# Kernel optimization log

Measured on AMD Instinct MI355X. Metric: run time of the kernel, lower is better.

## Reference

```python
import jax, jax.numpy as jnp
import numpy as np

TOP_K = 48
NUM_RBF = 16
MAX_REL = 32  # max_relative_feature
B, L = 2, 3072

# atom order in stacked tensor: N=0, Ca=1, C=2, O=3, Cb=4
_PAIRS = np.array([
    (0, 0), (2, 2), (3, 3), (4, 4), (1, 0), (1, 2), (1, 3), (1, 4),
    (0, 2), (0, 3), (0, 4), (4, 2), (4, 3), (3, 2), (0, 1), (2, 1),
    (3, 1), (4, 1), (2, 0), (3, 0), (4, 0), (2, 4), (3, 4), (2, 3)], dtype=np.int32)


def _rbf(D):
    # D [..., ] -> [..., NUM_RBF]
    mu = jnp.linspace(2.0, 22.0, NUM_RBF)
    sigma = (22.0 - 2.0) / NUM_RBF
    return jnp.exp(-(((D[..., None] - mu) / sigma) ** 2))


def setup_inputs() -> dict:
    key = jax.random.key(0)
    ks = jax.random.split(key, 8)
    X = jax.random.normal(ks[0], (B, L, 4, 3), dtype=jnp.float32) * 3.0
    mask = jnp.ones((B, L), dtype=jnp.float32)
    R_idx = jnp.sort(jax.random.randint(ks[1], (B, L), 0, 6144), axis=-1)
    chain_labels = jax.random.randint(ks[2], (B, L), 0, 4)
    pos_W = jax.random.normal(ks[3], (2 * MAX_REL + 2, 16), dtype=jnp.float32) * 0.1
    pos_b = jax.random.normal(ks[4], (16,), dtype=jnp.float32) * 0.02
    edge_W = jax.random.normal(ks[5], (16 + 25 * NUM_RBF, 128), dtype=jnp.float32) * 0.05
    ln_gamma = jnp.ones((128,), dtype=jnp.float32)
    ln_beta = jnp.zeros((128,), dtype=jnp.float32)
    return {"X": X, "mask": mask, "R_idx": R_idx, "chain_labels": chain_labels,
            "pos_W": pos_W, "pos_b": pos_b, "edge_W": edge_W,
            "ln_gamma": ln_gamma, "ln_beta": ln_beta}


def reference(X, mask, R_idx, chain_labels, pos_W, pos_b, edge_W, ln_gamma, ln_beta):
    # virtual Cb construction
    bvec = X[:, :, 1, :] - X[:, :, 0, :]
    cvec = X[:, :, 2, :] - X[:, :, 1, :]
    avec = jnp.cross(bvec, cvec)
    Ca = X[:, :, 1, :]
    Cb = -0.58273431 * avec + 0.56802827 * bvec - 0.54067466 * cvec + Ca
    atoms = jnp.stack([X[:, :, 0, :], Ca, X[:, :, 2, :], X[:, :, 3, :], Cb], axis=2)  # [B,L,5,3]

    # masked pairwise Ca distances + k smallest neighbors
    mask2d = mask[:, :, None] * mask[:, None, :]                        # [B,L,L]
    dX = Ca[:, :, None, :] - Ca[:, None, :, :]
    D = mask2d * jnp.sqrt(jnp.sum(dX ** 2, axis=-1) + 1e-6)
    D_max = jnp.max(D, axis=-1, keepdims=True)
    D_adjust = D + (1.0 - mask2d) * D_max
    k = min(TOP_K, X.shape[1])
    neg_vals, E_idx = jax.lax.top_k(-D_adjust, k)                       # [B,L,K]
    D_neighbors = -neg_vals

    # gather neighbor atom coords once: [B,L,K,5,3]
    atoms_nb = jax.vmap(lambda a, i: a[i])(atoms, E_idx)

    # 24 remaining atom-pair distances, restricted to neighbors (same math as
    # full cdist + gather since dist is computed per (i, E_idx[i,j]) pair)
    ai, bi = _PAIRS[:, 0], _PAIRS[:, 1]
    diff = atoms[:, :, None, ai, :] - atoms_nb[:, :, :, bi, :]          # [B,L,K,24,3]
    D24 = jnp.sqrt(jnp.sum(diff ** 2, axis=-1) + 1e-6)                  # [B,L,K,24]

    D_all = jnp.concatenate([D_neighbors[..., None], D24], axis=-1)    # [B,L,K,25]
    RBF_all = _rbf(D_all).reshape(D_all.shape[:3] + (25 * NUM_RBF,))   # [B,L,K,400]

    # positional encodings on neighbor offsets
    offset = R_idx[:, :, None] - R_idx[:, None, :]
    offset = jnp.take_along_axis(offset, E_idx, axis=2)                 # [B,L,K]
    same_chain = (chain_labels[:, :, None] - chain_labels[:, None, :] == 0).astype(jnp.int32)
    E_chains = jnp.take_along_axis(same_chain, E_idx, axis=2)           # [B,L,K]
    d = jnp.clip(offset + MAX_REL, 0, 2 * MAX_REL) * E_chains + (1 - E_chains) * (2 * MAX_REL + 1)
    E_positional = pos_W[d] + pos_b                                     # one-hot @ W == row gather

    E = jnp.concatenate([E_positional, RBF_all], axis=-1)              # [B,L,K,416]
    E = E @ edge_W                                                      # [B,L,K,128]
    mu = jnp.mean(E, axis=-1, keepdims=True)
    var = jnp.mean((E - mu) ** 2, axis=-1, keepdims=True)
    E = (E - mu) / jnp.sqrt(var + 1e-5) * ln_gamma + ln_beta
    return E, E_idx
```

## Files before the change

### kernel.cpp

```cpp
#include <hip/hip_runtime.h>
#include <hip/hip_bf16.h>
#include <stdint.h>
#include <math.h>

#define B_   2
#define L_   3072
#define K_   48
#define FDIM 416
#define NOUT 128
#define FRS8 424
#define NLUT 1920

__device__ const unsigned char PAIRC[24] = {
    0, 18, 27, 36, 8, 10, 11, 12, 2, 3, 4, 34, 35, 26,
    1, 17, 25, 33, 16, 24, 32, 20, 28, 19
};

typedef __attribute__((ext_vector_type(4))) float f32x4;

__global__ __launch_bounds__(256) void k_prep(const float* __restrict__ X,
                                              const float* __restrict__ mask,
                                              const float* __restrict__ edgeW,
                                              float* __restrict__ atoms,
                                              float* __restrict__ CaA4,
                                              unsigned char* __restrict__ Wt8,
                                              uint4* __restrict__ LUT)
{
    const int bid = blockIdx.x;
    if (bid < 52) {
        int idx4 = bid * 256 + threadIdx.x;
        int b = idx4 * 4;
        int lhi = (b >> 3) & 3;
        int l15 = (b >> 5) & 15;
        int nt  = (b >> 9) & 7;
        int kt  = b >> 12;
        int n = (nt >> 1) * 32 + 2 * l15 + (nt & 1);
        int kbase = kt * 32 + lhi * 8 + (b & 7);
        float v0 = edgeW[(kbase + 0) * NOUT + n];
        float v1 = edgeW[(kbase + 1) * NOUT + n];
        float v2 = edgeW[(kbase + 2) * NOUT + n];
        float v3 = edgeW[(kbase + 3) * NOUT + n];
        int w = __builtin_amdgcn_cvt_pk_fp8_f32(v0, v1, 0, false);
        w = __builtin_amdgcn_cvt_pk_fp8_f32(v2, v3, w, true);
        ((unsigned int*)Wt8)[idx4] = (unsigned int)w;
    } else if (bid < 60) {
        int e = (bid - 52) * 256 + threadIdx.x;
        if (e >= NLUT) return;
        float D = (float)e * 0.015625f;
        float z = (D - 2.0f) * 0.8f;
        unsigned int u[4];
        #pragma unroll
        for (int p = 0; p < 4; ++p) {
            float e0 = __expf(-(z * z)); z -= 1.0666667f;
            float e1 = __expf(-(z * z)); z -= 1.0666667f;
            float e2 = __expf(-(z * z)); z -= 1.0666667f;
            float e3 = __expf(-(z * z)); z -= 1.0666667f;
            int w = __builtin_amdgcn_cvt_pk_fp8_f32(e0, e1, 0, false);
            w = __builtin_amdgcn_cvt_pk_fp8_f32(e2, e3, w, true);
            u[p] = (unsigned int)w;
        }
        LUT[e] = make_uint4(u[0], u[1], u[2], u[3]);
    } else {
        int row = (bid - 60) * 256 + threadIdx.x;
        if (row >= B_ * L_) return;
        const float* x = X + row * 12;
        float nx = x[0], ny = x[1], nz = x[2];
        float cax = x[3], cay = x[4], caz = x[5];
        float cx = x[6], cy = x[7], cz = x[8];
        float ox = x[9], oy = x[10], oz = x[11];
        float bx = cax - nx, by = cay - ny, bz = caz - nz;
        float vx = cx - cax, vy = cy - cay, vz = cz - caz;
        float axv = by * vz - bz * vy;
        float ayv = bz * vx - bx * vz;
        float azv = bx * vy - by * vx;
        float cbx = -0.58273431f * axv + 0.56802827f * bx - 0.54067466f * vx + cax;
        float cby = -0.58273431f * ayv + 0.56802827f * by - 0.54067466f * vy + cay;
        float cbz = -0.58273431f * azv + 0.56802827f * bz - 0.54067466f * vz + caz;
        float* A = atoms + row * 16;
        A[0] = nx;  A[1] = ny;  A[2] = nz;
        A[3] = cax; A[4] = cay; A[5] = caz;
        A[6] = cx;  A[7] = cy;  A[8] = cz;
        A[9] = ox;  A[10] = oy; A[11] = oz;
        A[12] = cbx; A[13] = cby; A[14] = cbz;
        A[15] = 0.f;
        float4 c4 = make_float4(cax, cay, caz, mask[row]);
        *(float4*)(CaA4 + row * 4) = c4;
    }
}

__global__ __launch_bounds__(256) void k_topk(const float* __restrict__ CaA4,
                                              int* __restrict__ eidx,
                                              float* __restrict__ dnb,
                                              float* __restrict__ out_eidx_f)
{
    __shared__ __align__(16) unsigned int SH[3072];
    unsigned int* hist  = SH;
    unsigned int* candJ = SH + 2048;
    unsigned long long* candK = (unsigned long long*)SH;
    __shared__ unsigned int swave[4];
    __shared__ int sP;
    __shared__ unsigned int sCnt;

    const int row = blockIdx.x;
    const int b = row / L_;
    const int tid = threadIdx.x;
    const int lane = tid & 63;
    const int wv = tid >> 6;

    #pragma unroll
    for (int i = 0; i < 8; ++i) hist[tid + 256 * i] = 0;
    if (tid == 0) sCnt = 0;

    const float4 me = *(const float4*)(CaA4 + row * 4);
    const float4* Cb = (const float4*)(CaA4 + (size_t)b * L_ * 4);
    __syncthreads();

    unsigned int bits[12];
    #pragma unroll
    for (int m = 0; m < 12; ++m) {
        int j = tid + 256 * m;
        float4 nb = Cb[j];
        float dx = me.x - nb.x;
        float dy = me.y - nb.y;
        float dz = me.z - nb.z;
        float s = fmaf(dz, dz, fmaf(dy, dy, dx * dx)) + 1e-6f;
        bool live = (me.w * nb.w) != 0.0f;
        bits[m] = live ? __float_as_uint(s) : 0x7F800000u;
        atomicAdd(&hist[bits[m] >> 20], 1u);
    }
    __syncthreads();

    unsigned int loc[8];
    unsigned int s = 0;
    #pragma unroll
    for (int i = 0; i < 8; ++i) { loc[i] = hist[tid * 8 + i]; s += loc[i]; }
    unsigned int sc = s;
    #pragma unroll
    for (int off = 1; off < 64; off <<= 1) {
        unsigned int o = __shfl_up(sc, off);
        if (lane >= off) sc += o;
    }
    if (lane == 63) swave[wv] = sc;
    __syncthreads();
    unsigned int base = 0;
    #pragma unroll
    for (int w = 0; w < 4; ++w) if (w < wv) base += swave[w];
    unsigned int cum = base + sc - s;
    #pragma unroll
    for (int i = 0; i < 8; ++i) {
        unsigned int c = loc[i];
        if (cum < K_ && cum + c >= K_) sP = tid * 8 + i;
        cum += c;
    }
    __syncthreads();
    const unsigned int Pth = (unsigned int)sP + 2;

    #pragma unroll
    for (int m = 0; m < 12; ++m) {
        if ((bits[m] >> 20) <= Pth) {
            unsigned int pos = atomicAdd(&sCnt, 1u);
            if (pos < 1024) candJ[pos] = (unsigned)(tid + 256 * m);
        }
    }
    __syncthreads();
    int cnt = (int)sCnt;
    if (cnt > 1024) cnt = 1024;

    const double cax = (double)me.x, cay = (double)me.y, caz = (double)me.z;
    for (int i = tid; i < cnt; i += 256) {
        int j = (int)candJ[i];
        float4 nb = Cb[j];
        double dx = cax - (double)nb.x;
        double dy = cay - (double)nb.y;
        double dz = caz - (double)nb.z;
        double ss = dx * dx;
        ss = ss + dy * dy;
        ss = ss + dz * dz;
        ss = ss + 1e-6;
        float v = (float)sqrt(ss);
        candK[i] = ((unsigned long long)__float_as_uint(v) << 32) | (unsigned)j;
    }
    __syncthreads();

    if (cnt <= 64) {
        if (wv == 0) {
            unsigned long long k = (lane < cnt) ? candK[lane] : ~0ull;
            #pragma unroll
            for (int size = 2; size <= 64; size <<= 1) {
                #pragma unroll
                for (int stride = size >> 1; stride >= 1; stride >>= 1) {
                    unsigned long long o = __shfl_xor(k, stride);
                    bool low = (lane & stride) == 0;
                    bool up = (lane & size) == 0 || size == 64;
                    unsigned long long mn = k < o ? k : o;
                    unsigned long long mx = k < o ? o : k;
                    k = (low == up) ? mn : mx;
                }
            }
            if (lane < K_) {
                int gj = (int)(unsigned)(k & 0xffffffffu);
                eidx[row * K_ + lane] = gj;
                dnb[row * K_ + lane] = __uint_as_float((unsigned)(k >> 32));
                out_eidx_f[row * K_ + lane] = (float)gj;
            }
        }
    } else {
        int M2 = 128;
        while (M2 < cnt) M2 <<= 1;
        for (int i = cnt + tid; i < M2; i += 256) candK[i] = ~0ull;
        for (int size = 2; size <= M2; size <<= 1) {
            for (int stride = size >> 1; stride > 0; stride >>= 1) {
                __syncthreads();
                for (int i = tid; i < M2; i += 256) {
                    int p = i ^ stride;
                    if (p > i) {
                        unsigned long long a = candK[i];
                        unsigned long long c2 = candK[p];
                        bool up = ((i & size) == 0);
                        if ((a > c2) == up) { candK[i] = c2; candK[p] = a; }
                    }
                }
            }
        }
        __syncthreads();
        if (tid < K_) {
            unsigned long long g = candK[tid];
            int gj = (int)(unsigned)(g & 0xffffffffu);
            eidx[row * K_ + tid] = gj;
            dnb[row * K_ + tid] = __uint_as_float((unsigned)(g >> 32));
            out_eidx_f[row * K_ + tid] = (float)gj;
        }
    }
}

__global__ __launch_bounds__(256) void k_edge(const float* __restrict__ atoms,
                                              const int* __restrict__ eidx,
                                              const float* __restrict__ dnb,
                                              const int* __restrict__ Ridx,
                                              const int* __restrict__ chain,
                                              const float* __restrict__ posW,
                                              const float* __restrict__ posb,
                                              const unsigned char* __restrict__ Wt8,
                                              const uint4* __restrict__ LUT,
                                              const float* __restrict__ gamma,
                                              const float* __restrict__ beta,
                                              float* __restrict__ Eout)
{
    __shared__ __align__(16) unsigned char F8[K_ * FRS8];
    __shared__ __align__(16) float sOwn[16];
    __shared__ int   sE[K_];
    __shared__ float sDnb[K_];
    __shared__ int   sDpos[K_];
    __shared__ float Psum[K_][4];
    __shared__ float Psq[K_][4];

    const int row = blockIdx.x;
    const int b = row / L_;
    const int tid = threadIdx.x;

    if (tid < K_) {
        int j = eidx[row * K_ + tid];
        sE[tid] = j;
        sDnb[tid] = dnb[row * K_ + tid];
        int off = Ridx[row] - Ridx[b * L_ + j];
        int ch = (chain[row] == chain[b * L_ + j]) ? 1 : 0;
        sDpos[tid] = ch ? min(max(off + 32, 0), 64) : 65;
    } else if (tid < K_ + 4) {
        int part = tid - K_;
        *(float4*)(&sOwn[part * 4]) = *(const float4*)(atoms + (size_t)row * 16 + part * 4);
    }
    __syncthreads();

    if (tid < 240) {
        const int k = tid / 5;
        const int dd0 = tid - k * 5;
        const float* pj = atoms + ((size_t)b * L_ + sE[k]) * 16;
        unsigned char* Fk = F8 + k * FRS8;
        #pragma unroll
        for (int s5 = 0; s5 < 5; ++s5) {
            const int dd = dd0 + 5 * s5;
            float D;
            if (dd == 0) {
                D = sDnb[k];
            } else {
                int pr = PAIRC[dd - 1];
                int ai = pr >> 3, bi = pr & 7;
                float dx = sOwn[ai * 3 + 0] - pj[bi * 3 + 0];
                float dy = sOwn[ai * 3 + 1] - pj[bi * 3 + 1];
                float dz = sOwn[ai * 3 + 2] - pj[bi * 3 + 2];
                D = sqrtf(fmaf(dz, dz, fmaf(dy, dy, dx * dx)) + 1e-6f);
            }
            float Dc = fminf(D, 29.984375f);
            int idx = (int)fmaf(Dc, 64.0f, 0.5f);
            uint4 v = LUT[idx];
            *(uint4*)(Fk + 16 + dd * 16) = v;
        }
    }
    for (int s2 = tid; s2 < K_ * 16; s2 += 256) {
        int k = s2 >> 4, r = s2 & 15;
        float v = posW[sDpos[k] * 16 + r] + posb[r];
        int w = __builtin_amdgcn_cvt_pk_fp8_f32(v, v, 0, false);
        F8[k * FRS8 + r] = (unsigned char)(w & 0xff);
    }
    __syncthreads();

    const int lane = tid & 63;
    const int wv = tid >> 6;
    const int l15 = lane & 15;
    const int lhi = lane >> 4;

    f32x4 acc[3][2];
    #pragma unroll
    for (int mt = 0; mt < 3; ++mt)
        #pragma unroll
        for (int nn = 0; nn < 2; ++nn)
            acc[mt][nn] = (f32x4){0.f, 0.f, 0.f, 0.f};

    const unsigned char* wp = Wt8 + wv * 1024 + l15 * 32 + lhi * 8;
    long bc0 = *(const long*)(wp);
    long bc1 = *(const long*)(wp + 512);

    #pragma unroll 1
    for (int kt = 0; kt < 13; ++kt) {
        long bn0 = 0, bn1 = 0;
        if (kt < 12) {
            bn0 = *(const long*)(wp + (kt + 1) * 4096);
            bn1 = *(const long*)(wp + (kt + 1) * 4096 + 512);
        }
        const int k0 = kt * 32 + lhi * 8;
        long a0 = *(const long*)(F8 + (l15) * FRS8 + k0);
        long a1 = *(const long*)(F8 + (16 + l15) * FRS8 + k0);
        long a2 = *(const long*)(F8 + (32 + l15) * FRS8 + k0);
        acc[0][0] = __builtin_amdgcn_mfma_f32_16x16x32_fp8_fp8(a0, bc0, acc[0][0], 0, 0, 0);
        acc[0][1] = __builtin_amdgcn_mfma_f32_16x16x32_fp8_fp8(a0, bc1, acc[0][1], 0, 0, 0);
        acc[1][0] = __builtin_amdgcn_mfma_f32_16x16x32_fp8_fp8(a1, bc0, acc[1][0], 0, 0, 0);
        acc[1][1] = __builtin_amdgcn_mfma_f32_16x16x32_fp8_fp8(a1, bc1, acc[1][1], 0, 0, 0);
        acc[2][0] = __builtin_amdgcn_mfma_f32_16x16x32_fp8_fp8(a2, bc0, acc[2][0], 0, 0, 0);
        acc[2][1] = __builtin_amdgcn_mfma_f32_16x16x32_fp8_fp8(a2, bc1, acc[2][1], 0, 0, 0);
        bc0 = bn0;
        bc1 = bn1;
    }

    #pragma unroll
    for (int mt = 0; mt < 3; ++mt) {
        #pragma unroll
        for (int r = 0; r < 4; ++r) {
            float v0 = acc[mt][0][r], v1 = acc[mt][1][r];
            float sv = v0 + v1;
            float q = v0 * v0 + v1 * v1;
            #pragma unroll
            for (int off = 1; off < 16; off <<= 1) {
                sv += __shfl_xor(sv, off);
                q += __shfl_xor(q, off);
            }
            if (l15 == 0) {
                int er = mt * 16 + lhi * 4 + r;
                Psum[er][wv] = sv;
                Psq[er][wv] = q;
            }
        }
    }
    __syncthreads();

    const int c0p = wv * 32 + 2 * l15;
    float2 g2 = *(const float2*)(gamma + c0p);
    float2 b2 = *(const float2*)(beta + c0p);

    #pragma unroll
    for (int mt = 0; mt < 3; ++mt) {
        #pragma unroll
        for (int r = 0; r < 4; ++r) {
            int er = mt * 16 + lhi * 4 + r;
            float sv = Psum[er][0] + Psum[er][1] + Psum[er][2] + Psum[er][3];
            float q = Psq[er][0] + Psq[er][1] + Psq[er][2] + Psq[er][3];
            float mu = sv * (1.0f / 128.0f);
            float var = q * (1.0f / 128.0f) - mu * mu;
            float inv = 1.0f / sqrtf(var + 1e-5f);
            float2 o;
            o.x = (acc[mt][0][r] - mu) * inv * g2.x + b2.x;
            o.y = (acc[mt][1][r] - mu) * inv * g2.y + b2.y;
            *(float2*)(Eout + ((size_t)row * K_ + er) * 128 + c0p) = o;
        }
    }
}

extern "C" void kernel_launch(void* const* d_in, const int* in_sizes, int n_in,
                              void* d_out, int out_size, void* d_ws, size_t ws_size,
                              hipStream_t stream) {
    const float* X     = (const float*)d_in[0];
    const float* mask  = (const float*)d_in[1];
    const int*   Ridx  = (const int*)d_in[2];
    const int*   chain = (const int*)d_in[3];
    const float* posW  = (const float*)d_in[4];
    const float* posb  = (const float*)d_in[5];
    const float* edgeW = (const float*)d_in[6];
    const float* gamma = (const float*)d_in[7];
    const float* beta  = (const float*)d_in[8];

    float* out   = (float*)d_out;
    float* Eout  = out;
    float* EidxF = out + (size_t)B_ * L_ * K_ * NOUT;

    float* atoms = (float*)d_ws;
    float* CaA4  = atoms + (size_t)B_ * L_ * 16;
    int*   eidx  = (int*)(CaA4 + (size_t)B_ * L_ * 4);
    float* dnb   = (float*)(eidx + (size_t)B_ * L_ * K_);
    unsigned char* Wt8 = (unsigned char*)(dnb + (size_t)B_ * L_ * K_);
    uint4* LUT   = (uint4*)(Wt8 + 53248);

    hipLaunchKernelGGL(k_prep, dim3(60 + (B_ * L_ + 255) / 256), dim3(256), 0, stream,
                       X, mask, edgeW, atoms, CaA4, Wt8, LUT);
    hipLaunchKernelGGL(k_topk, dim3(B_ * L_), dim3(256), 0, stream,
                       CaA4, eidx, dnb, EidxF);
    hipLaunchKernelGGL(k_edge, dim3(B_ * L_), dim3(256), 0, stream,
                       atoms, eidx, dnb, Ridx, chain, posW, posb, Wt8, LUT, gamma, beta, Eout);
}
```

Baseline: 121.0 us.

## Process two rows per block in top-k and edge kernels

Both the top-k and edge kernels now handle two query rows per 256-thread block, halving the grid. In top-k, each loaded neighbour coordinate is reused for two distance computations and two histograms. In the edge kernel, each fp8 weight fragment loaded from global memory feeds six MFMA row tiles instead of three, halving weight traffic per row. The cost is more registers and shared memory per block, which may lower occupancy, and the candidate buffer per row shrinks from 1024 to 768 entries.

```diff
diff --git a/kernel.cpp b/kernel.cpp
--- a/kernel.cpp
+++ b/kernel.cpp
@@ -93,142 +93,197 @@
                                               float* __restrict__ dnb,
                                               float* __restrict__ out_eidx_f)
 {
-    __shared__ __align__(16) unsigned int SH[3072];
-    unsigned int* hist  = SH;
-    unsigned int* candJ = SH + 2048;
-    unsigned long long* candK = (unsigned long long*)SH;
+    __shared__ __align__(16) unsigned int SH[5632];
     __shared__ unsigned int swave[4];
-    __shared__ int sP;
-    __shared__ unsigned int sCnt;
-
-    const int row = blockIdx.x;
-    const int b = row / L_;
+    __shared__ int sP[2];
+    __shared__ unsigned int sCnt[2];
+
+    const int row0 = blockIdx.x * 2;
+    const int row1 = row0 + 1;
+    const int b = row0 / L_;
     const int tid = threadIdx.x;
     const int lane = tid & 63;
     const int wv = tid >> 6;
 
     #pragma unroll
-    for (int i = 0; i < 8; ++i) hist[tid + 256 * i] = 0;
-    if (tid == 0) sCnt = 0;
-
-    const float4 me = *(const float4*)(CaA4 + row * 4);
+    for (int i = 0; i < 16; ++i) SH[tid + 256 * i] = 0;
+    if (tid < 2) sCnt[tid] = 0;
+
+    const float4 me0 = *(const float4*)(CaA4 + row0 * 4);
+    const float4 me1 = *(const float4*)(CaA4 + row1 * 4);
     const float4* Cb = (const float4*)(CaA4 + (size_t)b * L_ * 4);
     __syncthreads();
 
-    unsigned int bits[12];
+    unsigned int bits0[12], bits1[12];
     #pragma unroll
     for (int m = 0; m < 12; ++m) {
         int j = tid + 256 * m;
         float4 nb = Cb[j];
-        float dx = me.x - nb.x;
-        float dy = me.y - nb.y;
-        float dz = me.z - nb.z;
-        float s = fmaf(dz, dz, fmaf(dy, dy, dx * dx)) + 1e-6f;
-        bool live = (me.w * nb.w) != 0.0f;
-        bits[m] = live ? __float_as_uint(s) : 0x7F800000u;
-        atomicAdd(&hist[bits[m] >> 20], 1u);
-    }
-    __syncthreads();
-
-    unsigned int loc[8];
-    unsigned int s = 0;
-    #pragma unroll
-    for (int i = 0; i < 8; ++i) { loc[i] = hist[tid * 8 + i]; s += loc[i]; }
-    unsigned int sc = s;
-    #pragma unroll
-    for (int off = 1; off < 64; off <<= 1) {
-        unsigned int o = __shfl_up(sc, off);
-        if (lane >= off) sc += o;
-    }
-    if (lane == 63) swave[wv] = sc;
-    __syncthreads();
-    unsigned int base = 0;
-    #pragma unroll
-    for (int w = 0; w < 4; ++w) if (w < wv) base += swave[w];
-    unsigned int cum = base + sc - s;
-    #pragma unroll
-    for (int i = 0; i < 8; ++i) {
-        unsigned int c = loc[i];
-        if (cum < K_ && cum + c >= K_) sP = tid * 8 + i;
-        cum += c;
-    }
-    __syncthreads();
-    const unsigned int Pth = (unsigned int)sP + 2;
-
+        float dx0 = me0.x - nb.x, dy0 = me0.y - nb.y, dz0 = me0.z - nb.z;
+        float s0 = fmaf(dz0, dz0, fmaf(dy0, dy0, dx0 * dx0)) + 1e-6f;
+        bits0[m] = ((me0.w * nb.w) != 0.0f) ? __float_as_uint(s0) : 0x7F800000u;
+        float dx1 = me1.x - nb.x, dy1 = me1.y - nb.y, dz1 = me1.z - nb.z;
+        float s1 = fmaf(dz1, dz1, fmaf(dy1, dy1, dx1 * dx1)) + 1e-6f;
+        bits1[m] = ((me1.w * nb.w) != 0.0f) ? __float_as_uint(s1) : 0x7F800000u;
+        atomicAdd(&SH[bits0[m] >> 20], 1u);
+        atomicAdd(&SH[2048 + (bits1[m] >> 20)], 1u);
+    }
+    __syncthreads();
+
+    #pragma unroll
+    for (int r2 = 0; r2 < 2; ++r2) {
+        unsigned int loc[8];
+        unsigned int s = 0;
+        #pragma unroll
+        for (int i = 0; i < 8; ++i) { loc[i] = SH[r2 * 2048 + tid * 8 + i]; s += loc[i]; }
+        unsigned int sc = s;
+        #pragma unroll
+        for (int off = 1; off < 64; off <<= 1) {
+            unsigned int o = __shfl_up(sc, off);
+            if (lane >= off) sc += o;
+        }
+        if (lane == 63) swave[wv] = sc;
+        __syncthreads();
+        unsigned int base = 0;
+        #pragma unroll
+        for (int w = 0; w < 4; ++w) if (w < wv) base += swave[w];
+        unsigned int cum = base + sc - s;
+        #pragma unroll
+        for (int i = 0; i < 8; ++i) {
+            unsigned int c = loc[i];
+            if (cum < K_ && cum + c >= K_) sP[r2] = tid * 8 + i;
+            cum += c;
+        }
+        __syncthreads();
+    }
+    const unsigned int Pth0 = (unsigned int)sP[0] + 2;
+    const unsigned int Pth1 = (unsigned int)sP[1] + 2;
+
+    unsigned int* candJ = SH + 4096;
     #pragma unroll
     for (int m = 0; m < 12; ++m) {
-        if ((bits[m] >> 20) <= Pth) {
-            unsigned int pos = atomicAdd(&sCnt, 1u);
-            if (pos < 1024) candJ[pos] = (unsigned)(tid + 256 * m);
-        }
-    }
-    __syncthreads();
-    int cnt = (int)sCnt;
-    if (cnt > 1024) cnt = 1024;
-
-    const double cax = (double)me.x, cay = (double)me.y, caz = (double)me.z;
-    for (int i = tid; i < cnt; i += 256) {
-        int j = (int)candJ[i];
-        float4 nb = Cb[j];
-        double dx = cax - (double)nb.x;
-        double dy = cay - (double)nb.y;
-        double dz = caz - (double)nb.z;
-        double ss = dx * dx;
-        ss = ss + dy * dy;
-        ss = ss + dz * dz;
-        ss = ss + 1e-6;
-        float v = (float)sqrt(ss);
-        candK[i] = ((unsigned long long)__float_as_uint(v) << 32) | (unsigned)j;
-    }
-    __syncthreads();
-
-    if (cnt <= 64) {
-        if (wv == 0) {
-            unsigned long long k = (lane < cnt) ? candK[lane] : ~0ull;
+        if ((bits0[m] >> 20) <= Pth0) {
+            unsigned int pos = atomicAdd(&sCnt[0], 1u);
+            if (pos < 768) candJ[pos] = (unsigned)(tid + 256 * m);
+        }
+        if ((bits1[m] >> 20) <= Pth1) {
+            unsigned int pos = atomicAdd(&sCnt[1], 1u);
+            if (pos < 768) candJ[768 + pos] = (unsigned)(tid + 256 * m);
+        }
+    }
+    __syncthreads();
+    int cnt0 = (int)sCnt[0]; if (cnt0 > 768) cnt0 = 768;
+    int cnt1 = (int)sCnt[1]; if (cnt1 > 768) cnt1 = 768;
+
+    unsigned long long* candK = (unsigned long long*)SH;
+    {
+        const double cax = (double)me0.x, cay = (double)me0.y, caz = (double)me0.z;
+        for (int i = tid; i < cnt0; i += 256) {
+            int j = (int)candJ[i];
+            float4 nb = Cb[j];
+            double dx = cax - (double)nb.x;
+            double dy = cay - (double)nb.y;
+            double dz = caz - (double)nb.z;
+            double ss = dx * dx;
+            ss = ss + dy * dy;
+            ss = ss + dz * dz;
+            ss = ss + 1e-6;
+            float v = (float)sqrt(ss);
+            candK[i] = ((unsigned long long)__float_as_uint(v) << 32) | (unsigned)j;
+        }
+    }
+    {
+        const double cax = (double)me1.x, cay = (double)me1.y, caz = (double)me1.z;
+        for (int i = tid; i < cnt1; i += 256) {
+            int j = (int)candJ[768 + i];
+            float4 nb = Cb[j];
+            double dx = cax - (double)nb.x;
+            double dy = cay - (double)nb.y;
+            double dz = caz - (double)nb.z;
+            double ss = dx * dx;
+            ss = ss + dy * dy;
+            ss = ss + dz * dz;
+            ss = ss + 1e-6;
+            float v = (float)sqrt(ss);
+            candK[1024 + i] = ((unsigned long long)__float_as_uint(v) << 32) | (unsigned)j;
+        }
+    }
+    __syncthreads();
+
+    const bool small0 = (cnt0 <= 64), small1 = (cnt1 <= 64);
+    if (small0 && wv == 0) {
+        unsigned long long k = (lane < cnt0) ? candK[lane] : ~0ull;
+        #pragma unroll
+        for (int size = 2; size <= 64; size <<= 1) {
             #pragma unroll
-            for (int size = 2; size <= 64; size <<= 1) {
-                #pragma unroll
-                for (int stride = size >> 1; stride >= 1; stride >>= 1) {
-                    unsigned long long o = __shfl_xor(k, stride);
-                    bool low = (lane & stride) == 0;
-                    bool up = (lane & size) == 0 || size == 64;
-                    unsigned long long mn = k < o ? k : o;
-                    unsigned long long mx = k < o ? o : k;
-                    k = (low == up) ? mn : mx;
-                }
-            }
-            if (lane < K_) {
-                int gj = (int)(unsigned)(k & 0xffffffffu);
-                eidx[row * K_ + lane] = gj;
-                dnb[row * K_ + lane] = __uint_as_float((unsigned)(k >> 32));
-                out_eidx_f[row * K_ + lane] = (float)gj;
-            }
-        }
-    } else {
+            for (int stride = size >> 1; stride >= 1; stride >>= 1) {
+                unsigned long long o = __shfl_xor(k, stride);
+                bool low = (lane & stride) == 0;
+                bool up = (lane & size) == 0 || size == 64;
+                unsigned long long mn = k < o ? k : o;
+                unsigned long long mx = k < o ? o : k;
+                k = (low == up) ? mn : mx;
+            }
+        }
+        if (lane < K_) {
+            int gj = (int)(unsigned)(k & 0xffffffffu);
+            eidx[row0 * K_ + lane] = gj;
+            dnb[row0 * K_ + lane] = __uint_as_float((unsigned)(k >> 32));
+            out_eidx_f[row0 * K_ + lane] = (float)gj;
+        }
+    }
+    if (small1 && wv == 1) {
+        unsigned long long k = (lane < cnt1) ? candK[1024 + lane] : ~0ull;
+        #pragma unroll
+        for (int size = 2; size <= 64; size <<= 1) {
+            #pragma unroll
+            for (int stride = size >> 1; stride >= 1; stride >>= 1) {
+                unsigned long long o = __shfl_xor(k, stride);
+                bool low = (lane & stride) == 0;
+                bool up = (lane & size) == 0 || size == 64;
+                unsigned long long mn = k < o ? k : o;
+                unsigned long long mx = k < o ? o : k;
+                k = (low == up) ? mn : mx;
+            }
+        }
+        if (lane < K_) {
+            int gj = (int)(unsigned)(k & 0xffffffffu);
+            eidx[row1 * K_ + lane] = gj;
+            dnb[row1 * K_ + lane] = __uint_as_float((unsigned)(k >> 32));
+            out_eidx_f[row1 * K_ + lane] = (float)gj;
+        }
+    }
+    #pragma unroll
+    for (int r2 = 0; r2 < 2; ++r2) {
+        int cnt = r2 ? cnt1 : cnt0;
+        bool small = r2 ? small1 : small0;
+        if (small) continue;
+        unsigned long long* ck = candK + r2 * 1024;
+        int rowg = r2 ? row1 : row0;
         int M2 = 128;
         while (M2 < cnt) M2 <<= 1;
-        for (int i = cnt + tid; i < M2; i += 256) candK[i] = ~0ull;
+        for (int i = cnt + tid; i < M2; i += 256) ck[i] = ~0ull;
         for (int size = 2; size <= M2; size <<= 1) {
             for (int stride = size >> 1; stride > 0; stride >>= 1) {
                 __syncthreads();
                 for (int i = tid; i < M2; i += 256) {
                     int p = i ^ stride;
                     if (p > i) {
-                        unsigned long long a = candK[i];
-                        unsigned long long c2 = candK[p];
+                        unsigned long long a = ck[i];
+                        unsigned long long c2 = ck[p];
                         bool up = ((i & size) == 0);
-                        if ((a > c2) == up) { candK[i] = c2; candK[p] = a; }
+                        if ((a > c2) == up) { ck[i] = c2; ck[p] = a; }
                     }
                 }
             }
         }
         __syncthreads();
         if (tid < K_) {
-            unsigned long long g = candK[tid];
+            unsigned long long g = ck[tid];
             int gj = (int)(unsigned)(g & 0xffffffffu);
-            eidx[row * K_ + tid] = gj;
-            dnb[row * K_ + tid] = __uint_as_float((unsigned)(g >> 32));
-            out_eidx_f[row * K_ + tid] = (float)gj;
+            eidx[rowg * K_ + tid] = gj;
+            dnb[rowg * K_ + tid] = __uint_as_float((unsigned)(g >> 32));
+            out_eidx_f[rowg * K_ + tid] = (float)gj;
         }
     }
 }
@@ -246,61 +301,70 @@
                                               const float* __restrict__ beta,
                                               float* __restrict__ Eout)
 {
-    __shared__ __align__(16) unsigned char F8[K_ * FRS8];
-    __shared__ __align__(16) float sOwn[16];
-    __shared__ int   sE[K_];
-    __shared__ float sDnb[K_];
-    __shared__ int   sDpos[K_];
-    __shared__ float Psum[K_][4];
-    __shared__ float Psq[K_][4];
-
-    const int row = blockIdx.x;
-    const int b = row / L_;
+    __shared__ __align__(16) unsigned char F8[96 * FRS8];
+    __shared__ __align__(16) float sOwn[2][16];
+    __shared__ int   sE[96];
+    __shared__ float sDnb[96];
+    __shared__ int   sDpos[96];
+    __shared__ float Psum[96][4];
+    __shared__ float Psq[96][4];
+
+    const int row0 = blockIdx.x * 2;
+    const int b = row0 / L_;
     const int tid = threadIdx.x;
 
-    if (tid < K_) {
-        int j = eidx[row * K_ + tid];
+    if (tid < 96) {
+        int r2 = (tid >= 48) ? 1 : 0;
+        int row = row0 + r2;
+        int kl = tid - r2 * 48;
+        int j = eidx[row * K_ + kl];
         sE[tid] = j;
-        sDnb[tid] = dnb[row * K_ + tid];
+        sDnb[tid] = dnb[row * K_ + kl];
         int off = Ridx[row] - Ridx[b * L_ + j];
         int ch = (chain[row] == chain[b * L_ + j]) ? 1 : 0;
         sDpos[tid] = ch ? min(max(off + 32, 0), 64) : 65;
-    } else if (tid < K_ + 4) {
-        int part = tid - K_;
-        *(float4*)(&sOwn[part * 4]) = *(const float4*)(atoms + (size_t)row * 16 + part * 4);
+    } else if (tid < 104) {
+        int part = tid - 96;
+        int r2 = part >> 2;
+        *(float4*)(&sOwn[r2][(part & 3) * 4]) =
+            *(const float4*)(atoms + (size_t)(row0 + r2) * 16 + (part & 3) * 4);
     }
     __syncthreads();
 
     if (tid < 240) {
         const int k = tid / 5;
         const int dd0 = tid - k * 5;
-        const float* pj = atoms + ((size_t)b * L_ + sE[k]) * 16;
-        unsigned char* Fk = F8 + k * FRS8;
-        #pragma unroll
-        for (int s5 = 0; s5 < 5; ++s5) {
-            const int dd = dd0 + 5 * s5;
-            float D;
-            if (dd == 0) {
-                D = sDnb[k];
-            } else {
-                int pr = PAIRC[dd - 1];
-                int ai = pr >> 3, bi = pr & 7;
-                float dx = sOwn[ai * 3 + 0] - pj[bi * 3 + 0];
-                float dy = sOwn[ai * 3 + 1] - pj[bi * 3 + 1];
-                float dz = sOwn[ai * 3 + 2] - pj[bi * 3 + 2];
-                D = sqrtf(fmaf(dz, dz, fmaf(dy, dy, dx * dx)) + 1e-6f);
-            }
-            float Dc = fminf(D, 29.984375f);
-            int idx = (int)fmaf(Dc, 64.0f, 0.5f);
-            uint4 v = LUT[idx];
-            *(uint4*)(Fk + 16 + dd * 16) = v;
-        }
-    }
-    for (int s2 = tid; s2 < K_ * 16; s2 += 256) {
-        int k = s2 >> 4, r = s2 & 15;
-        float v = posW[sDpos[k] * 16 + r] + posb[r];
+        #pragma unroll
+        for (int r2 = 0; r2 < 2; ++r2) {
+            const int e = r2 * 48 + k;
+            const float* pj = atoms + ((size_t)b * L_ + sE[e]) * 16;
+            unsigned char* Fk = F8 + e * FRS8;
+            #pragma unroll
+            for (int s5 = 0; s5 < 5; ++s5) {
+                const int dd = dd0 + 5 * s5;
+                float D;
+                if (dd == 0) {
+                    D = sDnb[e];
+                } else {
+                    int pr = PAIRC[dd - 1];
+                    int ai = pr >> 3, bi = pr & 7;
+                    float dx = sOwn[r2][ai * 3 + 0] - pj[bi * 3 + 0];
+                    float dy = sOwn[r2][ai * 3 + 1] - pj[bi * 3 + 1];
+                    float dz = sOwn[r2][ai * 3 + 2] - pj[bi * 3 + 2];
+                    D = sqrtf(fmaf(dz, dz, fmaf(dy, dy, dx * dx)) + 1e-6f);
+                }
+                float Dc = fminf(D, 29.984375f);
+                int idx = (int)fmaf(Dc, 64.0f, 0.5f);
+                uint4 v = LUT[idx];
+                *(uint4*)(Fk + 16 + dd * 16) = v;
+            }
+        }
+    }
+    for (int s2 = tid; s2 < 96 * 16; s2 += 256) {
+        int e = s2 >> 4, r = s2 & 15;
+        float v = posW[sDpos[e] * 16 + r] + posb[r];
         int w = __builtin_amdgcn_cvt_pk_fp8_f32(v, v, 0, false);
-        F8[k * FRS8 + r] = (unsigned char)(w & 0xff);
+        F8[e * FRS8 + r] = (unsigned char)(w & 0xff);
     }
     __syncthreads();
 
@@ -309,9 +373,9 @@
     const int l15 = lane & 15;
     const int lhi = lane >> 4;
 
-    f32x4 acc[3][2];
-    #pragma unroll
-    for (int mt = 0; mt < 3; ++mt)
+    f32x4 acc[6][2];
+    #pragma unroll
+    for (int mt = 0; mt < 6; ++mt)
         #pragma unroll
         for (int nn = 0; nn < 2; ++nn)
             acc[mt][nn] = (f32x4){0.f, 0.f, 0.f, 0.f};
@@ -328,21 +392,18 @@
             bn1 = *(const long*)(wp + (kt + 1) * 4096 + 512);
         }
         const int k0 = kt * 32 + lhi * 8;
-        long a0 = *(const long*)(F8 + (l15) * FRS8 + k0);
-        long a1 = *(const long*)(F8 + (16 + l15) * FRS8 + k0);
-        long a2 = *(const long*)(F8 + (32 + l15) * FRS8 + k0);
-        acc[0][0] = __builtin_amdgcn_mfma_f32_16x16x32_fp8_fp8(a0, bc0, acc[0][0], 0, 0, 0);
-        acc[0][1] = __builtin_amdgcn_mfma_f32_16x16x32_fp8_fp8(a0, bc1, acc[0][1], 0, 0, 0);
-        acc[1][0] = __builtin_amdgcn_mfma_f32_16x16x32_fp8_fp8(a1, bc0, acc[1][0], 0, 0, 0);
-        acc[1][1] = __builtin_amdgcn_mfma_f32_16x16x32_fp8_fp8(a1, bc1, acc[1][1], 0, 0, 0);
-        acc[2][0] = __builtin_amdgcn_mfma_f32_16x16x32_fp8_fp8(a2, bc0, acc[2][0], 0, 0, 0);
-        acc[2][1] = __builtin_amdgcn_mfma_f32_16x16x32_fp8_fp8(a2, bc1, acc[2][1], 0, 0, 0);
+        #pragma unroll
+        for (int mt = 0; mt < 6; ++mt) {
+            long a = *(const long*)(F8 + (mt * 16 + l15) * FRS8 + k0);
+            acc[mt][0] = __builtin_amdgcn_mfma_f32_16x16x32_fp8_fp8(a, bc0, acc[mt][0], 0, 0, 0);
+            acc[mt][1] = __builtin_amdgcn_mfma_f32_16x16x32_fp8_fp8(a, bc1, acc[mt][1], 0, 0, 0);
+        }
         bc0 = bn0;
         bc1 = bn1;
     }
 
     #pragma unroll
-    for (int mt = 0; mt < 3; ++mt) {
+    for (int mt = 0; mt < 6; ++mt) {
         #pragma unroll
         for (int r = 0; r < 4; ++r) {
             float v0 = acc[mt][0][r], v1 = acc[mt][1][r];
@@ -367,7 +428,7 @@
     float2 b2 = *(const float2*)(beta + c0p);
 
     #pragma unroll
-    for (int mt = 0; mt < 3; ++mt) {
+    for (int mt = 0; mt < 6; ++mt) {
         #pragma unroll
         for (int r = 0; r < 4; ++r) {
             int er = mt * 16 + lhi * 4 + r;
@@ -376,10 +437,12 @@
             float mu = sv * (1.0f / 128.0f);
             float var = q * (1.0f / 128.0f) - mu * mu;
             float inv = 1.0f / sqrtf(var + 1e-5f);
+            int row = row0 + (er >= 48 ? 1 : 0);
+            int kl = er & 47;
             float2 o;
             o.x = (acc[mt][0][r] - mu) * inv * g2.x + b2.x;
             o.y = (acc[mt][1][r] - mu) * inv * g2.y + b2.y;
-            *(float2*)(Eout + ((size_t)row * K_ + er) * 128 + c0p) = o;
+            *(float2*)(Eout + ((size_t)row * K_ + kl) * 128 + c0p) = o;
         }
     }
 }
@@ -410,8 +473,8 @@
 
     hipLaunchKernelGGL(k_prep, dim3(60 + (B_ * L_ + 255) / 256), dim3(256), 0, stream,
                        X, mask, edgeW, atoms, CaA4, Wt8, LUT);
-    hipLaunchKernelGGL(k_topk, dim3(B_ * L_), dim3(256), 0, stream,
+    hipLaunchKernelGGL(k_topk, dim3(B_ * L_ / 2), dim3(256), 0, stream,
                        CaA4, eidx, dnb, EidxF);
-    hipLaunchKernelGGL(k_edge, dim3(B_ * L_), dim3(256), 0, stream,
+    hipLaunchKernelGGL(k_edge, dim3(B_ * L_ / 2), dim3(256), 0, stream,
                        atoms, eidx, dnb, Ridx, chain, posW, posb, Wt8, LUT, gamma, beta, Eout);
 }
```

New measurement: 160.6 us. 1.33x slower.

## Split edge GEMM over eight waves with one N-tile per wave

Applied to the files above, without the earlier changes.

Doubles the k_edge block to 512 threads so each of eight waves computes a single 16-column output tile instead of two, halving per-wave accumulators and weight loads. Feature construction is respread over 480 threads, and the LayerNorm partial sums now reduce across eight waves. Output stores shrink from float2 to scalar with interleaved columns, which may hurt store coalescing. The intent is more latency hiding per row, at the cost of more synchronisation and shared-memory reduction work.

```diff
diff --git a/kernel.cpp b/kernel.cpp
--- a/kernel.cpp
+++ b/kernel.cpp
@@ -233,7 +233,7 @@
     }
 }
 
-__global__ __launch_bounds__(256) void k_edge(const float* __restrict__ atoms,
+__global__ __launch_bounds__(512) void k_edge(const float* __restrict__ atoms,
                                               const int* __restrict__ eidx,
                                               const float* __restrict__ dnb,
                                               const int* __restrict__ Ridx,
@@ -251,8 +251,8 @@
     __shared__ int   sE[K_];
     __shared__ float sDnb[K_];
     __shared__ int   sDpos[K_];
-    __shared__ float Psum[K_][4];
-    __shared__ float Psq[K_][4];
+    __shared__ float Psum[K_][8];
+    __shared__ float Psq[K_][8];
 
     const int row = blockIdx.x;
     const int b = row / L_;
@@ -271,14 +271,15 @@
     }
     __syncthreads();
 
-    if (tid < 240) {
-        const int k = tid / 5;
-        const int dd0 = tid - k * 5;
+    if (tid < 480) {
+        const int k = tid / 10;
+        const int dd0 = tid - k * 10;
         const float* pj = atoms + ((size_t)b * L_ + sE[k]) * 16;
         unsigned char* Fk = F8 + k * FRS8;
         #pragma unroll
-        for (int s5 = 0; s5 < 5; ++s5) {
-            const int dd = dd0 + 5 * s5;
+        for (int s3 = 0; s3 < 3; ++s3) {
+            const int dd = dd0 + 10 * s3;
+            if (dd >= 25) break;
             float D;
             if (dd == 0) {
                 D = sDnb[k];
@@ -296,7 +297,7 @@
             *(uint4*)(Fk + 16 + dd * 16) = v;
         }
     }
-    for (int s2 = tid; s2 < K_ * 16; s2 += 256) {
+    for (int s2 = tid; s2 < K_ * 16; s2 += 512) {
         int k = s2 >> 4, r = s2 & 15;
         float v = posW[sDpos[k] * 16 + r] + posb[r];
         int w = __builtin_amdgcn_cvt_pk_fp8_f32(v, v, 0, false);
@@ -309,45 +310,35 @@
     const int l15 = lane & 15;
     const int lhi = lane >> 4;
 
-    f32x4 acc[3][2];
+    f32x4 acc[3];
     #pragma unroll
     for (int mt = 0; mt < 3; ++mt)
-        #pragma unroll
-        for (int nn = 0; nn < 2; ++nn)
-            acc[mt][nn] = (f32x4){0.f, 0.f, 0.f, 0.f};
-
-    const unsigned char* wp = Wt8 + wv * 1024 + l15 * 32 + lhi * 8;
-    long bc0 = *(const long*)(wp);
-    long bc1 = *(const long*)(wp + 512);
+        acc[mt] = (f32x4){0.f, 0.f, 0.f, 0.f};
+
+    const unsigned char* wp = Wt8 + wv * 512 + l15 * 32 + lhi * 8;
+    long bc = *(const long*)(wp);
 
     #pragma unroll 1
     for (int kt = 0; kt < 13; ++kt) {
-        long bn0 = 0, bn1 = 0;
-        if (kt < 12) {
-            bn0 = *(const long*)(wp + (kt + 1) * 4096);
-            bn1 = *(const long*)(wp + (kt + 1) * 4096 + 512);
-        }
+        long bn = 0;
+        if (kt < 12) bn = *(const long*)(wp + (kt + 1) * 4096);
         const int k0 = kt * 32 + lhi * 8;
         long a0 = *(const long*)(F8 + (l15) * FRS8 + k0);
         long a1 = *(const long*)(F8 + (16 + l15) * FRS8 + k0);
         long a2 = *(const long*)(F8 + (32 + l15) * FRS8 + k0);
-        acc[0][0] = __builtin_amdgcn_mfma_f32_16x16x32_fp8_fp8(a0, bc0, acc[0][0], 0, 0, 0);
-        acc[0][1] = __builtin_amdgcn_mfma_f32_16x16x32_fp8_fp8(a0, bc1, acc[0][1], 0, 0, 0);
-        acc[1][0] = __builtin_amdgcn_mfma_f32_16x16x32_fp8_fp8(a1, bc0, acc[1][0], 0, 0, 0);
-        acc[1][1] = __builtin_amdgcn_mfma_f32_16x16x32_fp8_fp8(a1, bc1, acc[1][1], 0, 0, 0);
-        acc[2][0] = __builtin_amdgcn_mfma_f32_16x16x32_fp8_fp8(a2, bc0, acc[2][0], 0, 0, 0);
-        acc[2][1] = __builtin_amdgcn_mfma_f32_16x16x32_fp8_fp8(a2, bc1, acc[2][1], 0, 0, 0);
-        bc0 = bn0;
-        bc1 = bn1;
+        acc[0] = __builtin_amdgcn_mfma_f32_16x16x32_fp8_fp8(a0, bc, acc[0], 0, 0, 0);
+        acc[1] = __builtin_amdgcn_mfma_f32_16x16x32_fp8_fp8(a1, bc, acc[1], 0, 0, 0);
+        acc[2] = __builtin_amdgcn_mfma_f32_16x16x32_fp8_fp8(a2, bc, acc[2], 0, 0, 0);
+        bc = bn;
     }
 
     #pragma unroll
     for (int mt = 0; mt < 3; ++mt) {
         #pragma unroll
         for (int r = 0; r < 4; ++r) {
-            float v0 = acc[mt][0][r], v1 = acc[mt][1][r];
-            float sv = v0 + v1;
-            float q = v0 * v0 + v1 * v1;
+            float v0 = acc[mt][r];
+            float sv = v0;
+            float q = v0 * v0;
             #pragma unroll
             for (int off = 1; off < 16; off <<= 1) {
                 sv += __shfl_xor(sv, off);
@@ -362,24 +353,22 @@
     }
     __syncthreads();
 
-    const int c0p = wv * 32 + 2 * l15;
-    float2 g2 = *(const float2*)(gamma + c0p);
-    float2 b2 = *(const float2*)(beta + c0p);
+    const int c0 = (wv >> 1) * 32 + 2 * l15 + (wv & 1);
+    float g1 = gamma[c0];
+    float b1 = beta[c0];
 
     #pragma unroll
     for (int mt = 0; mt < 3; ++mt) {
         #pragma unroll
         for (int r = 0; r < 4; ++r) {
             int er = mt * 16 + lhi * 4 + r;
-            float sv = Psum[er][0] + Psum[er][1] + Psum[er][2] + Psum[er][3];
-            float q = Psq[er][0] + Psq[er][1] + Psq[er][2] + Psq[er][3];
+            float sv = 0.f, q = 0.f;
+            #pragma unroll
+            for (int w = 0; w < 8; ++w) { sv += Psum[er][w]; q += Psq[er][w]; }
             float mu = sv * (1.0f / 128.0f);
             float var = q * (1.0f / 128.0f) - mu * mu;
             float inv = 1.0f / sqrtf(var + 1e-5f);
-            float2 o;
-            o.x = (acc[mt][0][r] - mu) * inv * g2.x + b2.x;
-            o.y = (acc[mt][1][r] - mu) * inv * g2.y + b2.y;
-            *(float2*)(Eout + ((size_t)row * K_ + er) * 128 + c0p) = o;
+            Eout[((size_t)row * K_ + er) * 128 + c0] = (acc[mt][r] - mu) * inv * g1 + b1;
         }
     }
 }
@@ -412,6 +401,6 @@
                        X, mask, edgeW, atoms, CaA4, Wt8, LUT);
     hipLaunchKernelGGL(k_topk, dim3(B_ * L_), dim3(256), 0, stream,
                        CaA4, eidx, dnb, EidxF);
-    hipLaunchKernelGGL(k_edge, dim3(B_ * L_), dim3(256), 0, stream,
+    hipLaunchKernelGGL(k_edge, dim3(B_ * L_), dim3(512), 0, stream,
                        atoms, eidx, dnb, Ridx, chain, posW, posb, Wt8, LUT, gamma, beta, Eout);
 }
```

Result: slower. 154.8 us (+27.9%).
